# Kernel tuning notes

Measured on AMD Instinct MI355X. Metric: run time of the kernel, lower is better.

Reference implementation:

```python
import jax, jax.numpy as jnp
import numpy as np

OUT = 3      # pooled output size (fmap_size//4 = 14//4 = 3)
RATIO = 2    # roi_align sampling ratio (fixed; torchvision adaptive ratio for 14/3 bins is 2)
P = 20       # num_persons


def _bilinear(fm, y, x):
    # fm: [C,H,W]; y,x broadcastable coordinate grids. torchvision aligned=False semantics.
    C, H, W = fm.shape
    y, x = jnp.broadcast_arrays(y, x)
    valid = (y > -1.0) & (y < H) & (x > -1.0) & (x < W)
    y = jnp.clip(y, 0.0, H - 1.0)
    x = jnp.clip(x, 0.0, W - 1.0)
    y0 = jnp.floor(y).astype(jnp.int32)
    x0 = jnp.floor(x).astype(jnp.int32)
    y1 = jnp.minimum(y0 + 1, H - 1)
    x1 = jnp.minimum(x0 + 1, W - 1)
    ly = y - y0
    lx = x - x0
    hy = 1.0 - ly
    hx = 1.0 - lx
    v00 = fm[:, y0, x0]
    v01 = fm[:, y0, x1]
    v10 = fm[:, y1, x0]
    v11 = fm[:, y1, x1]
    val = hy * hx * v00 + hy * lx * v01 + ly * hx * v10 + ly * lx * v11
    return jnp.where(valid, val, 0.0)  # [C, ...]


def _roi_align_one(fm, box):
    # fm: [C,H,W], box: [4] = (x1,y1,x2,y2) in feature-map coords -> [C,OUT,OUT]
    x1, y1, x2, y2 = box
    bw = (x2 - x1) / OUT
    bh = (y2 - y1) / OUT
    off = (jnp.arange(OUT * RATIO, dtype=fm.dtype) + 0.5) / RATIO  # bin-unit offsets
    xs = x1 + off * bw
    ys = y1 + off * bh
    vals = _bilinear(fm, ys[:, None], xs[None, :])  # [C, OUT*RATIO, OUT*RATIO]
    C = fm.shape[0]
    return vals.reshape(C, OUT, RATIO, OUT, RATIO).mean(axis=(2, 4))


def setup_inputs() -> dict:
    key = jax.random.key(0)
    ks = jax.random.split(key, 8)
    B, N, NB, C, FS = 128, 8, 27, 1024, 14
    fmap = jax.random.normal(ks[0], (B, C, FS, FS), jnp.float32)
    # boxes in feature-map coordinates with x1<x2, y1<y2
    lo = jax.random.uniform(ks[1], (B, N, 2), jnp.float32) * 10.0
    ext = 2.0 + jax.random.uniform(ks[2], (B, N, 2), jnp.float32) * 4.0
    hi = jnp.minimum(lo + ext, float(FS))
    boxes = jnp.concatenate([lo, hi], axis=-1)  # [B,N,4] (x1,y1,x2,y2)
    # unique person ids per frame (scatter target indices)
    pids = jax.vmap(lambda k: jax.random.permutation(k, P)[:N])(jax.random.split(ks[3], B)).astype(jnp.int32)
    w1 = jax.random.normal(ks[4], (512, C), jnp.float32) * 0.02
    w2 = jax.random.normal(ks[5], (256, 512), jnp.float32) * 0.05
    fc1_w = jax.random.normal(ks[6], (1024, 256 * OUT * OUT), jnp.float32) * 0.02
    fc1_b = jnp.zeros((1024,), jnp.float32)
    fc2_w = jax.random.normal(ks[7], (27, 1024), jnp.float32) * 0.02
    fc2_b = jnp.zeros((27,), jnp.float32)
    return {"fmap": fmap, "boxes": boxes, "pids": pids, "w1": w1, "w2": w2,
            "fc1_w": fc1_w, "fc1_b": fc1_b, "fc2_w": fc2_w, "fc2_b": fc2_b}


def _forward(fmap, boxes, pids, w1, w2, fc1_w, fc1_b, fc2_w, fc2_b):
    B, N = boxes.shape[:2]
    # per-image, per-box ROI align: [B,N,C,3,3]
    roi = jax.vmap(jax.vmap(_roi_align_one, in_axes=(None, 0)), in_axes=(0, 0))(fmap, boxes)
    # behavior_conv: two bias-free 1x1 convs (no nonlinearity between)
    h = jnp.einsum('bnchw,oc->bnohw', roi, w1)
    h = jnp.einsum('bnchw,oc->bnohw', h, w2)  # [B,N,256,3,3]
    feat = h.reshape(B, N, -1)                # [B,N,2304]
    bidx = jnp.broadcast_to(jnp.arange(B)[:, None], (B, N))
    # scatter into behavior_tensor keyed by person id (unique pids per frame -> well-defined)
    bt = jnp.zeros((B, P, feat.shape[-1]), feat.dtype).at[bidx, pids].set(feat)
    mean_b = bt.mean(axis=0)                  # [P,2304] mean over batch
    cur = bt[bidx, pids]                      # [B,N,2304]
    diff = mean_b[pids] - cur
    # behavior_fc (dropout is identity at inference)
    h1 = jax.nn.relu(jnp.einsum('bnd,hd->bnh', diff, fc1_w) + fc1_b)
    return jnp.einsum('bnh,oh->bno', h1, fc2_w) + fc2_b  # [B,N,num_behaviors]


def reference(fmap, boxes, pids, w1, w2, fc1_w, fc1_b, fc2_w, fc2_b):
    # fmap is detached and roi_align runs under no_grad in the original
    return _forward(jax.lax.stop_gradient(fmap), jax.lax.stop_gradient(boxes), pids,
                    w1, w2, fc1_w, fc1_b, fc2_w, fc2_b)
```

## Files before the change

### kernel.cpp

```cpp
#include <hip/hip_runtime.h>
#include <hip/hip_bf16.h>
#include <cstddef>
#include <cstdint>

#define B_   128
#define N_   8
#define C_   1024
#define FS_  14
#define POS_ 196
#define P_   20
#define HWC_ 9
#define CMID_ 256
#define FEATD_ 2304
#define H1_  1024
#define O_   27
#define GROWS_ (B_*POS_)

typedef __attribute__((ext_vector_type(8))) short bf16x8;
typedef __attribute__((ext_vector_type(4))) float f32x4;

__device__ __forceinline__ void gld16(const void* g, void* l) {
    __builtin_amdgcn_global_load_lds(
        (const __attribute__((address_space(1))) unsigned int*)g,
        (__attribute__((address_space(3))) unsigned int*)l, 16, 0, 0);
}

__global__ __launch_bounds__(256) void wcombine_split_kernel(
    const float* __restrict__ w1,
    const float* __restrict__ w2,
    float* __restrict__ wpart)
{
    const int tid = threadIdx.x;
    const int tx = tid & 15, ty = tid >> 4;
    const int c0 = blockIdx.x * 64;
    const int o0 = blockIdx.y * 64;
    const int kb = blockIdx.z * 64;
    __shared__ __align__(16) float As[16][68];
    __shared__ __align__(16) float Bs[16][68];
    float acc[4][4] = {};
    for (int k0 = kb; k0 < kb + 64; k0 += 16) {
        for (int i = tid; i < 64 * 16; i += 256) {
            int k = i & 15, m = i >> 4;
            As[k][m] = w2[(size_t)(o0 + m) * 512 + k0 + k];
        }
        for (int i = tid; i < 64 * 16; i += 256) {
            int n = i & 63, k = i >> 6;
            Bs[k][n] = w1[(size_t)(k0 + k) * 1024 + c0 + n];
        }
        __syncthreads();
        #pragma unroll
        for (int k = 0; k < 16; ++k) {
            float4 a = *(const float4*)&As[k][ty * 4];
            float4 b = *(const float4*)&Bs[k][tx * 4];
            float av[4] = {a.x, a.y, a.z, a.w};
            float bv[4] = {b.x, b.y, b.z, b.w};
            #pragma unroll
            for (int i = 0; i < 4; ++i)
                #pragma unroll
                for (int j = 0; j < 4; ++j)
                    acc[i][j] += av[i] * bv[j];
        }
        __syncthreads();
    }
    float* dst = wpart + (size_t)blockIdx.z * (256 * 1024);
    for (int i = 0; i < 4; ++i) {
        float4 v = make_float4(acc[i][0], acc[i][1], acc[i][2], acc[i][3]);
        *(float4*)&dst[(size_t)(o0 + ty * 4 + i) * 1024 + c0 + tx * 4] = v;
    }
}

__global__ __launch_bounds__(256) void wc_reduce_kernel(
    const float* __restrict__ wpart, __hip_bfloat16* __restrict__ Wc)
{
    int idx = blockIdx.x * 256 + threadIdx.x;
    float s = 0.f;
    #pragma unroll
    for (int z = 0; z < 8; ++z) s += wpart[(size_t)z * (256 * 1024) + idx];
    Wc[idx] = __float2bfloat16(s);
}

__global__ __launch_bounds__(256, 4) void posgemm_kernel(
    const float* __restrict__ fmap,
    const __hip_bfloat16* __restrict__ Wc,
    __hip_bfloat16* __restrict__ G)
{
    const int tid = threadIdx.x;
    const int wave = tid >> 6, lane = tid & 63;
    const int m16 = lane & 15, quad = lane >> 4;
    const int r0 = blockIdx.x * 32;

    const int rs = r0 + (tid & 31);
    const int b_s = rs / 196;
    const int pos_s = rs - b_s * 196;
    const size_t abase = (size_t)b_s * (C_ * POS_) + pos_s;
    const int cg = (tid >> 5) * 8;

    __shared__ __align__(16) __hip_bfloat16 As[32 * 66];
    __shared__ __align__(16) __hip_bfloat16 Bs[256 * 64];

    f32x4 acc[2][4];
    #pragma unroll
    for (int i = 0; i < 2; ++i)
        #pragma unroll
        for (int j = 0; j < 4; ++j)
            acc[i][j] = (f32x4){0.f, 0.f, 0.f, 0.f};

    for (int k0 = 0; k0 < 1024; k0 += 64) {
        #pragma unroll
        for (int jj = 0; jj < 8; ++jj) {
            int q = (wave * 8 + jj) * 64 + lane;
            int mq = q >> 3, cq = q & 7;
            int csq = cq ^ (mq & 7);
            gld16(Wc + (size_t)mq * 1024 + k0 + csq * 8,
                  (char*)Bs + (size_t)(wave * 8 + jj) * 1024);
        }
        {
            const float* fp = fmap + abase + (size_t)(k0 + cg) * POS_;
            float f0 = fp[0];
            float f1 = fp[POS_];
            float f2 = fp[2 * POS_];
            float f3 = fp[3 * POS_];
            float f4 = fp[4 * POS_];
            float f5 = fp[5 * POS_];
            float f6 = fp[6 * POS_];
            float f7 = fp[7 * POS_];
            __hip_bfloat162 p0, p1, p2, p3;
            p0.x = __float2bfloat16(f0); p0.y = __float2bfloat16(f1);
            p1.x = __float2bfloat16(f2); p1.y = __float2bfloat16(f3);
            p2.x = __float2bfloat16(f4); p2.y = __float2bfloat16(f5);
            p3.x = __float2bfloat16(f6); p3.y = __float2bfloat16(f7);
            __hip_bfloat16* ap = &As[(tid & 31) * 66 + cg];
            *(__hip_bfloat162*)(ap)     = p0;
            *(__hip_bfloat162*)(ap + 2) = p1;
            *(__hip_bfloat162*)(ap + 4) = p2;
            *(__hip_bfloat162*)(ap + 6) = p3;
        }
        __syncthreads();
        #pragma unroll
        for (int ks = 0; ks < 2; ++ks) {
            bf16x8 af[2], bfv[4];
            #pragma unroll
            for (int i = 0; i < 2; ++i) {
                int m = i * 16 + m16;
                af[i] = *(const bf16x8*)&As[m * 66 + (ks * 4 + quad) * 8];
            }
            #pragma unroll
            for (int j = 0; j < 4; ++j) {
                int n = wave * 64 + j * 16 + m16;
                int cq2 = (ks * 4 + quad) ^ (n & 7);
                bfv[j] = *(const bf16x8*)&Bs[(n * 8 + cq2) * 8];
            }
            #pragma unroll
            for (int i = 0; i < 2; ++i)
                #pragma unroll
                for (int j = 0; j < 4; ++j)
                    acc[i][j] = __builtin_amdgcn_mfma_f32_16x16x32_bf16(
                        af[i], bfv[j], acc[i][j], 0, 0, 0);
        }
        __syncthreads();
    }

    #pragma unroll
    for (int i = 0; i < 2; ++i) {
        #pragma unroll
        for (int j = 0; j < 4; ++j) {
            int col = wave * 64 + j * 16 + m16;
            int rb = r0 + i * 16 + quad * 4;
            #pragma unroll
            for (int g = 0; g < 4; ++g)
                G[(size_t)(rb + g) * 256 + col] = __float2bfloat16(acc[i][j][g]);
        }
    }
}

__global__ __launch_bounds__(576) void roi2_kernel(
    const __hip_bfloat16* __restrict__ G,
    const float* __restrict__ boxes,
    float* __restrict__ feat)
{
    const int b = blockIdx.y;
    const int o0 = blockIdx.x * 64;
    const int tid = threadIdx.x;
    const int l = tid & 63;
    const int cell = tid >> 6;
    const int ch = cell / 3, cw = cell % 3;
    __shared__ __align__(16) __hip_bfloat16 Ls[POS_ * 64];

    for (int idx = tid; idx < POS_ * 8; idx += 576) {
        int p = idx >> 3, chunk = idx & 7;
        const uint4* src = (const uint4*)(G +
            ((size_t)(b * POS_ + p) * 256 + o0 + chunk * 8));
        *(uint4*)&Ls[p * 64 + chunk * 8] = *src;
    }
    __syncthreads();

    for (int n = 0; n < N_; ++n) {
        const float* bx = boxes + (size_t)(b * N_ + n) * 4;
        float x1 = bx[0], y1 = bx[1], x2 = bx[2], y2 = bx[3];
        float bw = (x2 - x1) * (1.0f / 3.0f);
        float bh = (y2 - y1) * (1.0f / 3.0f);
        float acc = 0.0f;
        #pragma unroll
        for (int si = 0; si < 2; ++si) {
            float yy = y1 + ((float)(2 * ch + si) + 0.5f) * 0.5f * bh;
            #pragma unroll
            for (int sj = 0; sj < 2; ++sj) {
                float xx = x1 + ((float)(2 * cw + sj) + 0.5f) * 0.5f * bw;
                bool valid = (yy > -1.0f) && (yy < (float)FS_) &&
                             (xx > -1.0f) && (xx < (float)FS_);
                float y = fminf(fmaxf(yy, 0.0f), (float)(FS_ - 1));
                float x = fminf(fmaxf(xx, 0.0f), (float)(FS_ - 1));
                int y0 = (int)floorf(y);
                int x0 = (int)floorf(x);
                int y1i = min(y0 + 1, FS_ - 1);
                int x1i = min(x0 + 1, FS_ - 1);
                float ly = y - (float)y0, lx = x - (float)x0;
                float hy = 1.0f - ly,     hx = 1.0f - lx;
                float v00 = __bfloat162float(Ls[(y0  * FS_ + x0 ) * 64 + l]);
                float v01 = __bfloat162float(Ls[(y0  * FS_ + x1i) * 64 + l]);
                float v10 = __bfloat162float(Ls[(y1i * FS_ + x0 ) * 64 + l]);
                float v11 = __bfloat162float(Ls[(y1i * FS_ + x1i) * 64 + l]);
                float val = hy * hx * v00 + hy * lx * v01 +
                            ly * hx * v10 + ly * lx * v11;
                acc += valid ? val : 0.0f;
            }
        }
        feat[(size_t)(b * N_ + n) * FEATD_ + cell * 256 + o0 + l] = acc * 0.25f;
    }
}

__global__ __launch_bounds__(256, 4) void fc1_gemm_kernel(
    const __hip_bfloat16* __restrict__ A,
    const __hip_bfloat16* __restrict__ Bm,
    const float* __restrict__ bias,
    float* __restrict__ C)
{
    const int tid = threadIdx.x;
    const int wave = tid >> 6, lane = tid & 63;
    const int r0 = blockIdx.y * 32, n0 = blockIdx.x * 64;
    const int wm = (wave >> 1) * 16, wn = (wave & 1) * 32;
    const int m16 = lane & 15, quad = lane >> 4;
    const int K = FEATD_;
    __shared__ __align__(16) __hip_bfloat16 As[32 * 64];
    __shared__ __align__(16) __hip_bfloat16 Bs[64 * 64];

    f32x4 acc[2];
    acc[0] = (f32x4){0.f, 0.f, 0.f, 0.f};
    acc[1] = (f32x4){0.f, 0.f, 0.f, 0.f};

    const int qa = wave * 64 + lane;
    const int msA = qa >> 3, csA = (qa & 7) ^ (msA & 7);
    const int qb1 = qa + 256;
    const int msB1 = qb1 >> 3, csB1 = (qb1 & 7) ^ (msB1 & 7);
    const size_t rA  = (size_t)(r0 + msA)  * K + csA  * 8;
    const size_t rB0 = (size_t)(n0 + msA)  * K + csA  * 8;
    const size_t rB1 = (size_t)(n0 + msB1) * K + csB1 * 8;

    for (int k0 = 0; k0 < K; k0 += 64) {
        gld16(A  + rA  + k0, &As[wave * 512]);
        gld16(Bm + rB0 + k0, &Bs[wave * 512]);
        gld16(Bm + rB1 + k0, &Bs[2048 + wave * 512]);
        __syncthreads();
        #pragma unroll
        for (int ks = 0; ks < 2; ++ks) {
            bf16x8 af, bfv[2];
            int m = wm + m16;
            int cp = (ks * 4 + quad) ^ (m & 7);
            af = *(const bf16x8*)&As[(m * 8 + cp) * 8];
            #pragma unroll
            for (int t = 0; t < 2; ++t) {
                int n = wn + t * 16 + m16;
                int cq = (ks * 4 + quad) ^ (n & 7);
                bfv[t] = *(const bf16x8*)&Bs[(n * 8 + cq) * 8];
            }
            #pragma unroll
            for (int j = 0; j < 2; ++j)
                acc[j] = __builtin_amdgcn_mfma_f32_16x16x32_bf16(
                    af, bfv[j], acc[j], 0, 0, 0);
        }
        __syncthreads();
    }

    #pragma unroll
    for (int j = 0; j < 2; ++j) {
        int col = n0 + wn + j * 16 + m16;
        int rbase = r0 + wm + quad * 4;
        float bv = bias[col];
        #pragma unroll
        for (int g = 0; g < 4; ++g) {
            int r = rbase + g;
            float v = acc[j][g] + bv;
            C[(size_t)r * H1_ + col] = v > 0.f ? v : 0.f;
        }
    }
}

__global__ __launch_bounds__(256) void fc1w_perm_kernel(
    const float* __restrict__ src, __hip_bfloat16* __restrict__ dst)
{
    int h = blockIdx.x;
    int tid = threadIdx.x;
    __shared__ float buf[FEATD_];
    const float* s = src + (size_t)h * FEATD_;
    #pragma unroll
    for (int it = 0; it < 9; ++it)
        buf[it * 256 + tid] = s[it * 256 + tid];
    __syncthreads();
    __hip_bfloat16* d = dst + (size_t)h * FEATD_;
    #pragma unroll
    for (int it = 0; it < 9; ++it) {
        int dd = it * 256 + tid;
        d[dd] = __float2bfloat16(buf[tid * HWC_ + it]);
    }
}

__global__ __launch_bounds__(64) void invmap_kernel(
    const int* __restrict__ pids, int* __restrict__ inv)
{
    int b = blockIdx.x;
    int p = threadIdx.x;
    if (p < P_) {
        int v = -1;
        for (int n = 0; n < N_; ++n)
            if (pids[b * N_ + n] == p) v = n;
        inv[b * P_ + p] = v;
    }
}

__global__ __launch_bounds__(256) void meanb_kernel(
    const float* __restrict__ feat, const int* __restrict__ inv,
    float* __restrict__ mean_b)
{
    int p = blockIdx.x;
    int d = blockIdx.y * 256 + threadIdx.x;
    float acc = 0.0f;
    #pragma unroll 4
    for (int b = 0; b < B_; ++b) {
        int n = inv[b * P_ + p];
        if (n >= 0) acc += feat[(size_t)(b * N_ + n) * FEATD_ + d];
    }
    mean_b[(size_t)p * FEATD_ + d] = acc * (1.0f / (float)B_);
}

__global__ __launch_bounds__(256) void diff_kernel(
    const float* __restrict__ feat, const float* __restrict__ mean_b,
    const int* __restrict__ pids, __hip_bfloat16* __restrict__ diff)
{
    int r = blockIdx.x;
    int pid = pids[r];
    const float* fr = feat + (size_t)r * FEATD_;
    const float* mr = mean_b + (size_t)pid * FEATD_;
    __hip_bfloat16* dr = diff + (size_t)r * FEATD_;
    for (int d = threadIdx.x; d < FEATD_; d += 256)
        dr[d] = __float2bfloat16(mr[d] - fr[d]);
}

__global__ __launch_bounds__(256) void fc2_kernel(
    const float* __restrict__ h1, const float* __restrict__ fc2_w,
    const float* __restrict__ fc2_b, float* __restrict__ out)
{
    int bn = blockIdx.x;
    int tid = threadIdx.x;
    __shared__ __align__(16) float row[H1_];
    __shared__ float partial[32][8];
    ((float4*)row)[tid] = ((const float4*)(h1 + (size_t)bn * H1_))[tid];
    __syncthreads();
    int o = tid >> 3, part = tid & 7;
    float acc = 0.0f;
    if (o < O_) {
        const float* wrow = fc2_w + (size_t)o * H1_ + part * 128;
        const float* hrow = row + part * 128;
        #pragma unroll 4
        for (int j = 0; j < 128; ++j) acc += hrow[j] * wrow[j];
    }
    partial[o][part] = acc;
    __syncthreads();
    if (part == 0 && o < O_) {
        float s = fc2_b[o];
        #pragma unroll
        for (int p = 0; p < 8; ++p) s += partial[o][p];
        out[(size_t)bn * O_ + o] = s;
    }
}

extern "C" void kernel_launch(void* const* d_in, const int* in_sizes, int n_in,
                              void* d_out, int out_size, void* d_ws, size_t ws_size,
                              hipStream_t stream) {
    const float* fmap  = (const float*)d_in[0];
    const float* boxes = (const float*)d_in[1];
    const int*   pids  = (const int*)  d_in[2];
    const float* w1    = (const float*)d_in[3];
    const float* w2    = (const float*)d_in[4];
    const float* fc1_w = (const float*)d_in[5];
    const float* fc1_b = (const float*)d_in[6];
    const float* fc2_w = (const float*)d_in[7];
    const float* fc2_b = (const float*)d_in[8];
    float* out = (float*)d_out;

    char* wsb = (char*)d_ws;
    __hip_bfloat16* Wc    = (__hip_bfloat16*)wsb;
    __hip_bfloat16* G     = Wc + 256 * 1024;
    __hip_bfloat16* fc1wp = G + (size_t)GROWS_ * 256;
    __hip_bfloat16* diffp = fc1wp + (size_t)H1_ * FEATD_;
    float* feat   = (float*)(diffp + (size_t)H1_ * FEATD_);
    float* mean_b = feat + (size_t)(B_ * N_) * FEATD_;
    float* h1     = mean_b + (size_t)P_ * FEATD_;
    int*   inv    = (int*)(h1 + (size_t)(B_ * N_) * H1_);
    float* wpart  = (float*)(inv + 128 * P_ + 64);

    hipLaunchKernelGGL(wcombine_split_kernel, dim3(16, 4, 8), dim3(256), 0, stream,
                       w1, w2, wpart);
    hipLaunchKernelGGL(wc_reduce_kernel, dim3(1024), dim3(256), 0, stream,
                       wpart, Wc);
    hipLaunchKernelGGL(posgemm_kernel, dim3(GROWS_ / 32), dim3(256), 0, stream,
                       fmap, Wc, G);
    hipLaunchKernelGGL(roi2_kernel, dim3(4, 128), dim3(576), 0, stream,
                       G, boxes, feat);
    hipLaunchKernelGGL(fc1w_perm_kernel, dim3(1024), dim3(256), 0, stream,
                       fc1_w, fc1wp);
    hipLaunchKernelGGL(invmap_kernel, dim3(128), dim3(64), 0, stream,
                       pids, inv);
    hipLaunchKernelGGL(meanb_kernel, dim3(20, 9), dim3(256), 0, stream,
                       feat, inv, mean_b);
    hipLaunchKernelGGL(diff_kernel, dim3(1024), dim3(256), 0, stream,
                       feat, mean_b, pids, diffp);
    hipLaunchKernelGGL(fc1_gemm_kernel, dim3(16, 32), dim3(256), 0, stream,
                       diffp, fc1wp, fc1_b, h1);
    hipLaunchKernelGGL(fc2_kernel, dim3(1024), dim3(256), 0, stream,
                       h1, fc2_w, fc2_b, out);
}
```

Measured before the change: 310.1 us.

## Double-buffer LDS tiles in posgemm and fc1 GEMM kernels

Adds ping-pong shared-memory buffers to both the position GEMM and the fc1 GEMM, so the global loads for the next K tile are issued before the MFMAs on the current tile and one barrier per iteration is dropped. In posgemm the K step shrinks from 64 to 32 with a new 4-chunk swizzle, and the fmap register loads are prefetched one step ahead and written to LDS after compute. This costs extra LDS and registers, which may lower occupancy, and the smaller posgemm K step means more iterations and barriers.

```diff
diff --git a/kernel.cpp b/kernel.cpp
--- a/kernel.cpp
+++ b/kernel.cpp
@@ -93,10 +93,19 @@
     const int b_s = rs / 196;
     const int pos_s = rs - b_s * 196;
     const size_t abase = (size_t)b_s * (C_ * POS_) + pos_s;
-    const int cg = (tid >> 5) * 8;
-
-    __shared__ __align__(16) __hip_bfloat16 As[32 * 66];
-    __shared__ __align__(16) __hip_bfloat16 Bs[256 * 64];
+    const int cg = (tid >> 5) * 4;
+
+    __shared__ __align__(16) __hip_bfloat16 As[2][32 * 34];
+    __shared__ __align__(16) __hip_bfloat16 Bs[2][256 * 32];
+
+    size_t bsrc[4];
+    #pragma unroll
+    for (int jj = 0; jj < 4; ++jj) {
+        int q = jj * 256 + tid;
+        int mq = q >> 2, cq = q & 3;
+        int csq = cq ^ ((mq >> 1) & 3);
+        bsrc[jj] = (size_t)mq * 1024 + csq * 8;
+    }
 
     f32x4 acc[2][4];
     #pragma unroll
@@ -105,50 +114,48 @@
         for (int j = 0; j < 4; ++j)
             acc[i][j] = (f32x4){0.f, 0.f, 0.f, 0.f};
 
-    for (int k0 = 0; k0 < 1024; k0 += 64) {
-        #pragma unroll
-        for (int jj = 0; jj < 8; ++jj) {
-            int q = (wave * 8 + jj) * 64 + lane;
-            int mq = q >> 3, cq = q & 7;
-            int csq = cq ^ (mq & 7);
-            gld16(Wc + (size_t)mq * 1024 + k0 + csq * 8,
-                  (char*)Bs + (size_t)(wave * 8 + jj) * 1024);
-        }
+    float fA[4];
+
+    {
+        const float* fp = fmap + abase + (size_t)cg * POS_;
+        fA[0] = fp[0]; fA[1] = fp[POS_]; fA[2] = fp[2 * POS_]; fA[3] = fp[3 * POS_];
+        #pragma unroll
+        for (int jj = 0; jj < 4; ++jj)
+            gld16(Wc + bsrc[jj],
+                  (char*)&Bs[0][0] + (size_t)(jj * 256 + wave * 64) * 16);
+        __hip_bfloat162 p0, p1;
+        p0.x = __float2bfloat16(fA[0]); p0.y = __float2bfloat16(fA[1]);
+        p1.x = __float2bfloat16(fA[2]); p1.y = __float2bfloat16(fA[3]);
+        __hip_bfloat16* ap = &As[0][(tid & 31) * 34 + cg];
+        *(__hip_bfloat162*)(ap)     = p0;
+        *(__hip_bfloat162*)(ap + 2) = p1;
+    }
+    __syncthreads();
+
+    for (int t = 0; t < 31; ++t) {
+        const int cur = t & 1, nxt = cur ^ 1;
+        const int k1 = (t + 1) * 32;
+
+        const float* fp = fmap + abase + (size_t)(k1 + cg) * POS_;
+        fA[0] = fp[0]; fA[1] = fp[POS_]; fA[2] = fp[2 * POS_]; fA[3] = fp[3 * POS_];
+
+        #pragma unroll
+        for (int jj = 0; jj < 4; ++jj)
+            gld16(Wc + bsrc[jj] + k1,
+                  (char*)&Bs[nxt][0] + (size_t)(jj * 256 + wave * 64) * 16);
+
         {
-            const float* fp = fmap + abase + (size_t)(k0 + cg) * POS_;
-            float f0 = fp[0];
-            float f1 = fp[POS_];
-            float f2 = fp[2 * POS_];
-            float f3 = fp[3 * POS_];
-            float f4 = fp[4 * POS_];
-            float f5 = fp[5 * POS_];
-            float f6 = fp[6 * POS_];
-            float f7 = fp[7 * POS_];
-            __hip_bfloat162 p0, p1, p2, p3;
-            p0.x = __float2bfloat16(f0); p0.y = __float2bfloat16(f1);
-            p1.x = __float2bfloat16(f2); p1.y = __float2bfloat16(f3);
-            p2.x = __float2bfloat16(f4); p2.y = __float2bfloat16(f5);
-            p3.x = __float2bfloat16(f6); p3.y = __float2bfloat16(f7);
-            __hip_bfloat16* ap = &As[(tid & 31) * 66 + cg];
-            *(__hip_bfloat162*)(ap)     = p0;
-            *(__hip_bfloat162*)(ap + 2) = p1;
-            *(__hip_bfloat162*)(ap + 4) = p2;
-            *(__hip_bfloat162*)(ap + 6) = p3;
-        }
-        __syncthreads();
-        #pragma unroll
-        for (int ks = 0; ks < 2; ++ks) {
             bf16x8 af[2], bfv[4];
             #pragma unroll
             for (int i = 0; i < 2; ++i) {
                 int m = i * 16 + m16;
-                af[i] = *(const bf16x8*)&As[m * 66 + (ks * 4 + quad) * 8];
+                af[i] = *(const bf16x8*)&As[cur][m * 34 + quad * 8];
             }
             #pragma unroll
             for (int j = 0; j < 4; ++j) {
                 int n = wave * 64 + j * 16 + m16;
-                int cq2 = (ks * 4 + quad) ^ (n & 7);
-                bfv[j] = *(const bf16x8*)&Bs[(n * 8 + cq2) * 8];
+                int cq2 = quad ^ ((n >> 1) & 3);
+                bfv[j] = *(const bf16x8*)&Bs[cur][(n * 4 + cq2) * 8];
             }
             #pragma unroll
             for (int i = 0; i < 2; ++i)
@@ -157,7 +164,38 @@
                     acc[i][j] = __builtin_amdgcn_mfma_f32_16x16x32_bf16(
                         af[i], bfv[j], acc[i][j], 0, 0, 0);
         }
+
+        {
+            __hip_bfloat162 p0, p1;
+            p0.x = __float2bfloat16(fA[0]); p0.y = __float2bfloat16(fA[1]);
+            p1.x = __float2bfloat16(fA[2]); p1.y = __float2bfloat16(fA[3]);
+            __hip_bfloat16* ap = &As[nxt][(tid & 31) * 34 + cg];
+            *(__hip_bfloat162*)(ap)     = p0;
+            *(__hip_bfloat162*)(ap + 2) = p1;
+        }
         __syncthreads();
+    }
+
+    {
+        const int cur = 1;
+        bf16x8 af[2], bfv[4];
+        #pragma unroll
+        for (int i = 0; i < 2; ++i) {
+            int m = i * 16 + m16;
+            af[i] = *(const bf16x8*)&As[cur][m * 34 + quad * 8];
+        }
+        #pragma unroll
+        for (int j = 0; j < 4; ++j) {
+            int n = wave * 64 + j * 16 + m16;
+            int cq2 = quad ^ ((n >> 1) & 3);
+            bfv[j] = *(const bf16x8*)&Bs[cur][(n * 4 + cq2) * 8];
+        }
+        #pragma unroll
+        for (int i = 0; i < 2; ++i)
+            #pragma unroll
+            for (int j = 0; j < 4; ++j)
+                acc[i][j] = __builtin_amdgcn_mfma_f32_16x16x32_bf16(
+                    af[i], bfv[j], acc[i][j], 0, 0, 0);
     }
 
     #pragma unroll
@@ -241,8 +279,8 @@
     const int wm = (wave >> 1) * 16, wn = (wave & 1) * 32;
     const int m16 = lane & 15, quad = lane >> 4;
     const int K = FEATD_;
-    __shared__ __align__(16) __hip_bfloat16 As[32 * 64];
-    __shared__ __align__(16) __hip_bfloat16 Bs[64 * 64];
+    __shared__ __align__(16) __hip_bfloat16 As[2][32 * 64];
+    __shared__ __align__(16) __hip_bfloat16 Bs[2][64 * 64];
 
     f32x4 acc[2];
     acc[0] = (f32x4){0.f, 0.f, 0.f, 0.f};
@@ -256,22 +294,28 @@
     const size_t rB0 = (size_t)(n0 + msA)  * K + csA  * 8;
     const size_t rB1 = (size_t)(n0 + msB1) * K + csB1 * 8;
 
-    for (int k0 = 0; k0 < K; k0 += 64) {
-        gld16(A  + rA  + k0, &As[wave * 512]);
-        gld16(Bm + rB0 + k0, &Bs[wave * 512]);
-        gld16(Bm + rB1 + k0, &Bs[2048 + wave * 512]);
-        __syncthreads();
+    gld16(A  + rA,  &As[0][wave * 512]);
+    gld16(Bm + rB0, &Bs[0][wave * 512]);
+    gld16(Bm + rB1, &Bs[0][2048 + wave * 512]);
+    __syncthreads();
+
+    for (int t = 0; t < 35; ++t) {
+        const int cur = t & 1, nxt = cur ^ 1;
+        const int k1 = (t + 1) * 64;
+        gld16(A  + rA  + k1, &As[nxt][wave * 512]);
+        gld16(Bm + rB0 + k1, &Bs[nxt][wave * 512]);
+        gld16(Bm + rB1 + k1, &Bs[nxt][2048 + wave * 512]);
         #pragma unroll
         for (int ks = 0; ks < 2; ++ks) {
             bf16x8 af, bfv[2];
             int m = wm + m16;
             int cp = (ks * 4 + quad) ^ (m & 7);
-            af = *(const bf16x8*)&As[(m * 8 + cp) * 8];
-            #pragma unroll
-            for (int t = 0; t < 2; ++t) {
-                int n = wn + t * 16 + m16;
+            af = *(const bf16x8*)&As[cur][(m * 8 + cp) * 8];
+            #pragma unroll
+            for (int tt = 0; tt < 2; ++tt) {
+                int n = wn + tt * 16 + m16;
                 int cq = (ks * 4 + quad) ^ (n & 7);
-                bfv[t] = *(const bf16x8*)&Bs[(n * 8 + cq) * 8];
+                bfv[tt] = *(const bf16x8*)&Bs[cur][(n * 8 + cq) * 8];
             }
             #pragma unroll
             for (int j = 0; j < 2; ++j)
@@ -279,6 +323,24 @@
                     af, bfv[j], acc[j], 0, 0, 0);
         }
         __syncthreads();
+    }
+
+    #pragma unroll
+    for (int ks = 0; ks < 2; ++ks) {
+        bf16x8 af, bfv[2];
+        int m = wm + m16;
+        int cp = (ks * 4 + quad) ^ (m & 7);
+        af = *(const bf16x8*)&As[1][(m * 8 + cp) * 8];
+        #pragma unroll
+        for (int tt = 0; tt < 2; ++tt) {
+            int n = wn + tt * 16 + m16;
+            int cq = (ks * 4 + quad) ^ (n & 7);
+            bfv[tt] = *(const bf16x8*)&Bs[1][(n * 8 + cq) * 8];
+        }
+        #pragma unroll
+        for (int j = 0; j < 2; ++j)
+            acc[j] = __builtin_amdgcn_mfma_f32_16x16x32_bf16(
+                af, bfv[j], acc[j], 0, 0, 0);
     }
 
     #pragma unroll
```

Result: slower. 332.0 us (+7.0%).

## Pool ROIs from raw feature map before applying combined channel projection

Applied to the files above, without the earlier changes.

Reorders the pipeline so ROI-align bilinear pooling runs directly on the fp32 feature map per 64-channel slice, writing bf16 pooled rows, then a tiled MFMA GEMM applies the combined 1024->256 projection to the pooled rows only. This shrinks the projection GEMM from every spatial position to only the pooled cells. In exchange, it writes a larger bf16 intermediate and adds a separate pooling pass that stages the fmap through LDS.

```diff
diff --git a/kernel.cpp b/kernel.cpp
--- a/kernel.cpp
+++ b/kernel.cpp
@@ -14,7 +14,7 @@
 #define FEATD_ 2304
 #define H1_  1024
 #define O_   27
-#define GROWS_ (B_*POS_)
+#define PROWS_ (B_*N_*HWC_)
 
 typedef __attribute__((ext_vector_type(8))) short bf16x8;
 typedef __attribute__((ext_vector_type(4))) float f32x4;
@@ -79,153 +79,142 @@
     Wc[idx] = __float2bfloat16(s);
 }
 
-__global__ __launch_bounds__(256, 4) void posgemm_kernel(
+#define CCH_  64
+#define LSTR_ 197
+__global__ __launch_bounds__(256, 3) void roipool_kernel(
     const float* __restrict__ fmap,
-    const __hip_bfloat16* __restrict__ Wc,
-    __hip_bfloat16* __restrict__ G)
-{
+    const float* __restrict__ boxes,
+    __hip_bfloat16* __restrict__ pooled)
+{
+    const int b  = blockIdx.y;
+    const int c0 = blockIdx.x * CCH_;
     const int tid = threadIdx.x;
-    const int wave = tid >> 6, lane = tid & 63;
-    const int m16 = lane & 15, quad = lane >> 4;
-    const int r0 = blockIdx.x * 32;
-
-    const int rs = r0 + (tid & 31);
-    const int b_s = rs / 196;
-    const int pos_s = rs - b_s * 196;
-    const size_t abase = (size_t)b_s * (C_ * POS_) + pos_s;
-    const int cg = (tid >> 5) * 8;
-
-    __shared__ __align__(16) __hip_bfloat16 As[32 * 66];
-    __shared__ __align__(16) __hip_bfloat16 Bs[256 * 64];
-
-    f32x4 acc[2][4];
-    #pragma unroll
-    for (int i = 0; i < 2; ++i)
-        #pragma unroll
-        for (int j = 0; j < 4; ++j)
-            acc[i][j] = (f32x4){0.f, 0.f, 0.f, 0.f};
-
-    for (int k0 = 0; k0 < 1024; k0 += 64) {
-        #pragma unroll
-        for (int jj = 0; jj < 8; ++jj) {
-            int q = (wave * 8 + jj) * 64 + lane;
-            int mq = q >> 3, cq = q & 7;
-            int csq = cq ^ (mq & 7);
-            gld16(Wc + (size_t)mq * 1024 + k0 + csq * 8,
-                  (char*)Bs + (size_t)(wave * 8 + jj) * 1024);
-        }
-        {
-            const float* fp = fmap + abase + (size_t)(k0 + cg) * POS_;
-            float f0 = fp[0];
-            float f1 = fp[POS_];
-            float f2 = fp[2 * POS_];
-            float f3 = fp[3 * POS_];
-            float f4 = fp[4 * POS_];
-            float f5 = fp[5 * POS_];
-            float f6 = fp[6 * POS_];
-            float f7 = fp[7 * POS_];
-            __hip_bfloat162 p0, p1, p2, p3;
-            p0.x = __float2bfloat16(f0); p0.y = __float2bfloat16(f1);
-            p1.x = __float2bfloat16(f2); p1.y = __float2bfloat16(f3);
-            p2.x = __float2bfloat16(f4); p2.y = __float2bfloat16(f5);
-            p3.x = __float2bfloat16(f6); p3.y = __float2bfloat16(f7);
-            __hip_bfloat16* ap = &As[(tid & 31) * 66 + cg];
-            *(__hip_bfloat162*)(ap)     = p0;
-            *(__hip_bfloat162*)(ap + 2) = p1;
-            *(__hip_bfloat162*)(ap + 4) = p2;
-            *(__hip_bfloat162*)(ap + 6) = p3;
-        }
-        __syncthreads();
-        #pragma unroll
-        for (int ks = 0; ks < 2; ++ks) {
-            bf16x8 af[2], bfv[4];
-            #pragma unroll
-            for (int i = 0; i < 2; ++i) {
-                int m = i * 16 + m16;
-                af[i] = *(const bf16x8*)&As[m * 66 + (ks * 4 + quad) * 8];
-            }
-            #pragma unroll
-            for (int j = 0; j < 4; ++j) {
-                int n = wave * 64 + j * 16 + m16;
-                int cq2 = (ks * 4 + quad) ^ (n & 7);
-                bfv[j] = *(const bf16x8*)&Bs[(n * 8 + cq2) * 8];
-            }
-            #pragma unroll
-            for (int i = 0; i < 2; ++i)
-                #pragma unroll
-                for (int j = 0; j < 4; ++j)
-                    acc[i][j] = __builtin_amdgcn_mfma_f32_16x16x32_bf16(
-                        af[i], bfv[j], acc[i][j], 0, 0, 0);
-        }
-        __syncthreads();
-    }
-
-    #pragma unroll
-    for (int i = 0; i < 2; ++i) {
-        #pragma unroll
-        for (int j = 0; j < 4; ++j) {
-            int col = wave * 64 + j * 16 + m16;
-            int rb = r0 + i * 16 + quad * 4;
-            #pragma unroll
-            for (int g = 0; g < 4; ++g)
-                G[(size_t)(rb + g) * 256 + col] = __float2bfloat16(acc[i][j][g]);
-        }
-    }
-}
-
-__global__ __launch_bounds__(576) void roi2_kernel(
-    const __hip_bfloat16* __restrict__ G,
-    const float* __restrict__ boxes,
-    float* __restrict__ feat)
-{
-    const int b = blockIdx.y;
-    const int o0 = blockIdx.x * 64;
-    const int tid = threadIdx.x;
-    const int l = tid & 63;
-    const int cell = tid >> 6;
-    const int ch = cell / 3, cw = cell % 3;
-    __shared__ __align__(16) __hip_bfloat16 Ls[POS_ * 64];
-
-    for (int idx = tid; idx < POS_ * 8; idx += 576) {
-        int p = idx >> 3, chunk = idx & 7;
-        const uint4* src = (const uint4*)(G +
-            ((size_t)(b * POS_ + p) * 256 + o0 + chunk * 8));
-        *(uint4*)&Ls[p * 64 + chunk * 8] = *src;
+    __shared__ float Ls[CCH_ * LSTR_];
+
+    const float* src = fmap + ((size_t)b * C_ + c0) * POS_;
+    for (int i = tid; i < CCH_ * 49; i += 256) {
+        int c = i / 49, ch = i - c * 49;
+        float4 v = *(const float4*)(src + (size_t)c * POS_ + ch * 4);
+        float* dst = &Ls[c * LSTR_ + ch * 4];
+        dst[0] = v.x; dst[1] = v.y; dst[2] = v.z; dst[3] = v.w;
     }
     __syncthreads();
 
-    for (int n = 0; n < N_; ++n) {
-        const float* bx = boxes + (size_t)(b * N_ + n) * 4;
+    const int cl = tid & 63;
+    const int ng = tid >> 6;
+    const float* lsc = &Ls[cl * LSTR_];
+
+    #pragma unroll
+    for (int nn = 0; nn < 2; ++nn) {
+        const int n = ng * 2 + nn;
+        const float* bx = boxes + ((size_t)b * N_ + n) * 4;
         float x1 = bx[0], y1 = bx[1], x2 = bx[2], y2 = bx[3];
         float bw = (x2 - x1) * (1.0f / 3.0f);
         float bh = (y2 - y1) * (1.0f / 3.0f);
-        float acc = 0.0f;
-        #pragma unroll
-        for (int si = 0; si < 2; ++si) {
-            float yy = y1 + ((float)(2 * ch + si) + 0.5f) * 0.5f * bh;
-            #pragma unroll
-            for (int sj = 0; sj < 2; ++sj) {
-                float xx = x1 + ((float)(2 * cw + sj) + 0.5f) * 0.5f * bw;
-                bool valid = (yy > -1.0f) && (yy < (float)FS_) &&
-                             (xx > -1.0f) && (xx < (float)FS_);
-                float y = fminf(fmaxf(yy, 0.0f), (float)(FS_ - 1));
-                float x = fminf(fmaxf(xx, 0.0f), (float)(FS_ - 1));
-                int y0 = (int)floorf(y);
-                int x0 = (int)floorf(x);
-                int y1i = min(y0 + 1, FS_ - 1);
-                int x1i = min(x0 + 1, FS_ - 1);
-                float ly = y - (float)y0, lx = x - (float)x0;
-                float hy = 1.0f - ly,     hx = 1.0f - lx;
-                float v00 = __bfloat162float(Ls[(y0  * FS_ + x0 ) * 64 + l]);
-                float v01 = __bfloat162float(Ls[(y0  * FS_ + x1i) * 64 + l]);
-                float v10 = __bfloat162float(Ls[(y1i * FS_ + x0 ) * 64 + l]);
-                float v11 = __bfloat162float(Ls[(y1i * FS_ + x1i) * 64 + l]);
-                float val = hy * hx * v00 + hy * lx * v01 +
-                            ly * hx * v10 + ly * lx * v11;
-                acc += valid ? val : 0.0f;
+        __hip_bfloat16* prow = pooled +
+            (size_t)((b * N_ + n) * HWC_) * C_ + c0 + cl;
+        #pragma unroll
+        for (int cell = 0; cell < 9; ++cell) {
+            const int chh = cell / 3, cww = cell % 3;
+            float acc = 0.0f;
+            #pragma unroll
+            for (int si = 0; si < 2; ++si) {
+                float yy = y1 + ((float)(2 * chh + si) + 0.5f) * 0.5f * bh;
+                #pragma unroll
+                for (int sj = 0; sj < 2; ++sj) {
+                    float xx = x1 + ((float)(2 * cww + sj) + 0.5f) * 0.5f * bw;
+                    bool valid = (yy > -1.0f) && (yy < (float)FS_) &&
+                                 (xx > -1.0f) && (xx < (float)FS_);
+                    float y = fminf(fmaxf(yy, 0.0f), (float)(FS_ - 1));
+                    float x = fminf(fmaxf(xx, 0.0f), (float)(FS_ - 1));
+                    int y0 = (int)floorf(y);
+                    int x0 = (int)floorf(x);
+                    int y1i = min(y0 + 1, FS_ - 1);
+                    int x1i = min(x0 + 1, FS_ - 1);
+                    float ly = y - (float)y0, lx = x - (float)x0;
+                    float hy = 1.0f - ly,     hx = 1.0f - lx;
+                    float v00 = lsc[y0  * FS_ + x0 ];
+                    float v01 = lsc[y0  * FS_ + x1i];
+                    float v10 = lsc[y1i * FS_ + x0 ];
+                    float v11 = lsc[y1i * FS_ + x1i];
+                    float val = hy * hx * v00 + hy * lx * v01 +
+                                ly * hx * v10 + ly * lx * v11;
+                    acc += valid ? val : 0.0f;
+                }
             }
-        }
-        feat[(size_t)(b * N_ + n) * FEATD_ + cell * 256 + o0 + l] = acc * 0.25f;
+            prow[(size_t)cell * C_] = __float2bfloat16(acc * 0.25f);
+        }
+    }
+}
+
+__global__ __launch_bounds__(256, 4) void pooledgemm_kernel(
+    const __hip_bfloat16* __restrict__ A,
+    const __hip_bfloat16* __restrict__ Bm,
+    float* __restrict__ Cout)
+{
+    const int tid = threadIdx.x;
+    const int wave = tid >> 6, lane = tid & 63;
+    const int r0 = blockIdx.y * 64, n0 = blockIdx.x * 64;
+    const int wm = (wave >> 1) * 32, wn = (wave & 1) * 32;
+    const int m16 = lane & 15, quad = lane >> 4;
+    const int K = C_;
+    __shared__ __align__(16) __hip_bfloat16 As[64 * 64];
+    __shared__ __align__(16) __hip_bfloat16 Bs[64 * 64];
+
+    f32x4 acc[2][2];
+    #pragma unroll
+    for (int i = 0; i < 2; ++i)
+        #pragma unroll
+        for (int j = 0; j < 2; ++j)
+            acc[i][j] = (f32x4){0.f, 0.f, 0.f, 0.f};
+
+    const int qa = wave * 64 + lane;
+    const int ms0 = qa >> 3, cs0 = (qa & 7) ^ (ms0 & 7);
+    const int qb1 = qa + 256;
+    const int ms1 = qb1 >> 3, cs1 = (qb1 & 7) ^ (ms1 & 7);
+    const size_t rA0 = (size_t)(r0 + ms0) * K + cs0 * 8;
+    const size_t rA1 = (size_t)(r0 + ms1) * K + cs1 * 8;
+    const size_t rB0 = (size_t)(n0 + ms0) * K + cs0 * 8;
+    const size_t rB1 = (size_t)(n0 + ms1) * K + cs1 * 8;
+
+    for (int k0 = 0; k0 < K; k0 += 64) {
+        gld16(A  + rA0 + k0, &As[wave * 512]);
+        gld16(Bm + rB0 + k0, &Bs[wave * 512]);
+        gld16(A  + rA1 + k0, &As[2048 + wave * 512]);
+        gld16(Bm + rB1 + k0, &Bs[2048 + wave * 512]);
+        __syncthreads();
+        #pragma unroll
+        for (int ks = 0; ks < 2; ++ks) {
+            bf16x8 af[2], bfv[2];
+            #pragma unroll
+            for (int t = 0; t < 2; ++t) {
+                int m = wm + t * 16 + m16;
+                int cp = (ks * 4 + quad) ^ (m & 7);
+                af[t] = *(const bf16x8*)&As[(m * 8 + cp) * 8];
+                int n = wn + t * 16 + m16;
+                int cq = (ks * 4 + quad) ^ (n & 7);
+                bfv[t] = *(const bf16x8*)&Bs[(n * 8 + cq) * 8];
+            }
+            #pragma unroll
+            for (int i = 0; i < 2; ++i)
+                #pragma unroll
+                for (int j = 0; j < 2; ++j)
+                    acc[i][j] = __builtin_amdgcn_mfma_f32_16x16x32_bf16(
+                        af[i], bfv[j], acc[i][j], 0, 0, 0);
+        }
+        __syncthreads();
+    }
+
+    #pragma unroll
+    for (int i = 0; i < 2; ++i) {
+        #pragma unroll
+        for (int j = 0; j < 2; ++j) {
+            int col = n0 + wn + j * 16 + m16;
+            int rbase = r0 + wm + i * 16 + quad * 4;
+            #pragma unroll
+            for (int g = 0; g < 4; ++g)
+                Cout[(size_t)(rbase + g) * 256 + col] = acc[i][j][g];
+        }
     }
 }
 
@@ -398,10 +387,10 @@
     float* out = (float*)d_out;
 
     char* wsb = (char*)d_ws;
-    __hip_bfloat16* Wc    = (__hip_bfloat16*)wsb;
-    __hip_bfloat16* G     = Wc + 256 * 1024;
-    __hip_bfloat16* fc1wp = G + (size_t)GROWS_ * 256;
-    __hip_bfloat16* diffp = fc1wp + (size_t)H1_ * FEATD_;
+    __hip_bfloat16* Wc     = (__hip_bfloat16*)wsb;
+    __hip_bfloat16* pooled = Wc + 256 * 1024;
+    __hip_bfloat16* fc1wp  = pooled + (size_t)PROWS_ * C_;
+    __hip_bfloat16* diffp  = fc1wp + (size_t)H1_ * FEATD_;
     float* feat   = (float*)(diffp + (size_t)H1_ * FEATD_);
     float* mean_b = feat + (size_t)(B_ * N_) * FEATD_;
     float* h1     = mean_b + (size_t)P_ * FEATD_;
@@ -412,10 +401,10 @@
                        w1, w2, wpart);
     hipLaunchKernelGGL(wc_reduce_kernel, dim3(1024), dim3(256), 0, stream,
                        wpart, Wc);
-    hipLaunchKernelGGL(posgemm_kernel, dim3(GROWS_ / 32), dim3(256), 0, stream,
-                       fmap, Wc, G);
-    hipLaunchKernelGGL(roi2_kernel, dim3(4, 128), dim3(576), 0, stream,
-                       G, boxes, feat);
+    hipLaunchKernelGGL(roipool_kernel, dim3(16, 128), dim3(256), 0, stream,
+                       fmap, boxes, pooled);
+    hipLaunchKernelGGL(pooledgemm_kernel, dim3(4, 144), dim3(256), 0, stream,
+                       pooled, Wc, feat);
     hipLaunchKernelGGL(fc1w_perm_kernel, dim3(1024), dim3(256), 0, stream,
                        fc1_w, fc1wp);
     hipLaunchKernelGGL(invmap_kernel, dim3(128), dim3(64), 0, stream,
```

New measurement: 300.1 us. 3.2% less time.
